# Kernel tuning notes

Hardware: AMD Instinct MI355X
Metric: run time of the kernel (lower is better)

The kernel has to match this reference:

```python
import jax, jax.numpy as jnp
import numpy as np

D_MODEL = 768
H = 12
D_FF = 3072
EPS = 1e-6


def _layernorm(x, alpha, bias):
    # torch.std default is Bessel-corrected (ddof=1); denom is (std + eps)
    mean = jnp.mean(x, axis=-1, keepdims=True)
    var = jnp.sum((x - mean) ** 2, axis=-1, keepdims=True) / (x.shape[-1] - 1)
    std = jnp.sqrt(var)
    return alpha * (x - mean) / (std + EPS) + bias


def _linear(x, w, b):
    # torch nn.Linear: y = x @ W.T + b, W is [out, in]
    return jnp.einsum('...i,oi->...o', x, w) + b


def setup_inputs() -> dict:
    key = jax.random.key(0)
    ks = jax.random.split(key, 16)
    B, S = 8, 1024
    sc = 1.0 / np.sqrt(D_MODEL)
    inp = {
        'x': jax.random.normal(ks[0], (B, S, D_MODEL), dtype=jnp.float32),
        'mask': jax.random.randint(ks[1], (B, 1, 1, S), 0, 2, dtype=jnp.int32),
        'wq': jax.random.normal(ks[2], (D_MODEL, D_MODEL), dtype=jnp.float32) * sc,
        'bq': jnp.zeros((D_MODEL,), jnp.float32),
        'wk': jax.random.normal(ks[3], (D_MODEL, D_MODEL), dtype=jnp.float32) * sc,
        'bk': jnp.zeros((D_MODEL,), jnp.float32),
        'wv': jax.random.normal(ks[4], (D_MODEL, D_MODEL), dtype=jnp.float32) * sc,
        'bv': jnp.zeros((D_MODEL,), jnp.float32),
        'wo': jax.random.normal(ks[5], (D_MODEL, D_MODEL), dtype=jnp.float32) * sc,
        'bo': jnp.zeros((D_MODEL,), jnp.float32),
        'ln1_a': jnp.ones((D_MODEL,), jnp.float32),
        'ln1_b': jnp.zeros((D_MODEL,), jnp.float32),
        'ln2_a': jnp.ones((D_MODEL,), jnp.float32),
        'ln2_b': jnp.zeros((D_MODEL,), jnp.float32),
        'w1': jax.random.normal(ks[6], (D_FF, D_MODEL), dtype=jnp.float32) * sc,
        'b1': jnp.zeros((D_FF,), jnp.float32),
        'w2': jax.random.normal(ks[7], (D_MODEL, D_FF), dtype=jnp.float32) * (1.0 / np.sqrt(D_FF)),
        'b2': jnp.zeros((D_MODEL,), jnp.float32),
    }
    return inp


def reference(x, mask, wq, bq, wk, bk, wv, bv, wo, bo,
              ln1_a, ln1_b, ln2_a, ln2_b, w1, b1, w2, b2):
    B, S, _ = x.shape
    d_k = D_MODEL // H

    # --- residual 1: pre-LN self-attention (dropout identity at eval) ---
    xn = _layernorm(x, ln1_a, ln1_b)
    q = _linear(xn, wq, bq).reshape(B, S, H, d_k).transpose(0, 2, 1, 3)
    k = _linear(xn, wk, bk).reshape(B, S, H, d_k).transpose(0, 2, 1, 3)
    v = _linear(xn, wv, bv).reshape(B, S, H, d_k).transpose(0, 2, 1, 3)

    scores = jnp.einsum('bhqd,bhkd->bhqk', q, k) / jnp.sqrt(jnp.float32(d_k))
    # faithful quirk: masked positions set to 1e-9, NOT -inf
    scores = jnp.where(mask == 0, jnp.float32(1e-9), scores)
    attn = jax.nn.softmax(scores, axis=-1)
    ctx = jnp.einsum('bhqk,bhkd->bhqd', attn, v)
    ctx = ctx.transpose(0, 2, 1, 3).reshape(B, S, D_MODEL)
    x = x + _linear(ctx, wo, bo)

    # --- residual 2: pre-LN feed-forward ---
    xn = _layernorm(x, ln2_a, ln2_b)
    ff = _linear(jax.nn.relu(_linear(xn, w1, b1)), w2, b2)
    return x + ff
```

## Files before the change

### kernel.cpp

```cpp
#include <hip/hip_runtime.h>
#include <stdint.h>

#define D_MODEL 768
#define D_FF    3072
#define NH      12
#define DK      64
#define BB      8
#define SS      1024
#define NTOK    (BB*SS)
#define QST     2304

typedef float          f32x4  __attribute__((ext_vector_type(4)));
typedef __bf16         bf16x8 __attribute__((ext_vector_type(8)));
typedef unsigned short us8v   __attribute__((ext_vector_type(8)));
typedef unsigned short us4v   __attribute__((ext_vector_type(4)));

__device__ __forceinline__ unsigned short f2b(float f) {
  unsigned int u = __builtin_bit_cast(unsigned int, f);
  u = (u + 0x7fffu + ((u >> 16) & 1u)) >> 16;
  return (unsigned short)u;
}
__device__ __forceinline__ float b2f(unsigned short h) {
  unsigned int u = ((unsigned int)h) << 16;
  return __builtin_bit_cast(float, u);
}
__device__ __forceinline__ float exp2a(float x) {
  float r; asm("v_exp_f32 %0, %1" : "=v"(r) : "v"(x)); return r;
}
__device__ __forceinline__ unsigned int cvtpk(float lo, float hi) {
  unsigned int r;
  asm("v_cvt_pk_bf16_f32 %0, %1, %2" : "=v"(r) : "v"(lo), "v"(hi));
  return r;
}

__global__ __launch_bounds__(256) void cast_kernel(const float* __restrict__ src,
                                                   unsigned short* __restrict__ dst,
                                                   int n4) {
  int i = blockIdx.x * 256 + threadIdx.x;
  if (i >= n4) return;
  const float4* s4 = (const float4*)src;
  float4 f = s4[i];
  us4v o; o.x = f2b(f.x); o.y = f2b(f.y); o.z = f2b(f.z); o.w = f2b(f.w);
  *(us4v*)(dst + (size_t)i * 4) = o;
}

__global__ __launch_bounds__(256) void ln_kernel(const float* __restrict__ x,
                                                 const float* __restrict__ ga,
                                                 const float* __restrict__ gb,
                                                 unsigned short* __restrict__ y) {
  int row = blockIdx.x;
  const float* xr = x + (size_t)row * D_MODEL;
  int t = threadIdx.x, w = t >> 6, l = t & 63;
  float v0 = xr[t], v1 = xr[t + 256], v2 = xr[t + 512];
  float s = v0 + v1 + v2;
  #pragma unroll
  for (int off = 32; off; off >>= 1) s += __shfl_xor(s, off);
  __shared__ float red[4];
  __shared__ float stats[2];
  if (l == 0) red[w] = s;
  __syncthreads();
  if (t == 0) stats[0] = (red[0] + red[1] + red[2] + red[3]) * (1.0f / 768.0f);
  __syncthreads();
  float mean = stats[0];
  float d0 = v0 - mean, d1 = v1 - mean, d2 = v2 - mean;
  float ss = d0 * d0 + d1 * d1 + d2 * d2;
  #pragma unroll
  for (int off = 32; off; off >>= 1) ss += __shfl_xor(ss, off);
  __syncthreads();
  if (l == 0) red[w] = ss;
  __syncthreads();
  if (t == 0) {
    float tot = red[0] + red[1] + red[2] + red[3];
    stats[1] = 1.0f / (sqrtf(tot * (1.0f / 767.0f)) + 1e-6f);
  }
  __syncthreads();
  float inv = stats[1];
  unsigned short* yr = y + (size_t)row * D_MODEL;
  yr[t]       = f2b(ga[t]       * (d0 * inv) + gb[t]);
  yr[t + 256] = f2b(ga[t + 256] * (d1 * inv) + gb[t + 256]);
  yr[t + 512] = f2b(ga[t + 512] * (d2 * inv) + gb[t + 512]);
}

#define GLDS(g, l) __builtin_amdgcn_global_load_lds( \
    (__attribute__((address_space(1))) const void*)(g), \
    (__attribute__((address_space(3))) void*)(l), 16, 0, 0)

template<int BN>
__global__ __launch_bounds__(256) void gemm_t(
    const unsigned short* __restrict__ A,
    const unsigned short* __restrict__ W,
    const float* __restrict__ biasA,
    const float* __restrict__ biasB,
    const float* __restrict__ biasC,
    int segw,
    const float* __restrict__ resid,
    float* __restrict__ outF,
    unsigned short* __restrict__ outB,
    int M, int N, int K, int relu) {
  constexpr int WC = (BN == 128) ? 2 : 1;
  constexpr int MF = (BN == 128) ? 4 : 2;
  constexpr int NF = 4;
  __shared__ unsigned short As[128 * 32];
  __shared__ unsigned short Bs[BN * 32];
  int t = threadIdx.x;
  int w = t >> 6, l = t & 63;
  int brow = blockIdx.x * 128;
  int bcol = blockIdx.y * BN;
  int wr = (w / WC) * (MF * 16);
  int wc = (w % WC) * (NF * 16);

  const unsigned short* ga0 = A + (size_t)(brow + (t >> 2)) * K + (t & 3) * 8;
  const unsigned short* ga1 = ga0 + (size_t)64 * K;
  const unsigned short* gb0 = W + (size_t)(bcol + (t >> 2)) * K + (t & 3) * 8;
  const unsigned short* gb1 = gb0 + (size_t)64 * K;

  f32x4 acc[MF][NF];
  #pragma unroll
  for (int m = 0; m < MF; m++)
    #pragma unroll
    for (int n = 0; n < NF; n++)
      acc[m][n] = (f32x4){0.f, 0.f, 0.f, 0.f};

  int arow = wr + (l & 15);
  int bcw  = wc + (l & 15);
  int kk   = (l >> 4) * 8;

  for (int k0 = 0; k0 < K; k0 += 32) {
    GLDS(ga0 + k0, As + t * 8);
    GLDS(ga1 + k0, As + 2048 + t * 8);
    GLDS(gb0 + k0, Bs + t * 8);
    if (BN == 128) GLDS(gb1 + k0, Bs + 2048 + t * 8);
    __syncthreads();
    bf16x8 af[MF], bfv[NF];
    #pragma unroll
    for (int m = 0; m < MF; m++)
      af[m] = *(const bf16x8*)(As + (arow + m * 16) * 32 + kk);
    #pragma unroll
    for (int n = 0; n < NF; n++)
      bfv[n] = *(const bf16x8*)(Bs + (bcw + n * 16) * 32 + kk);
    #pragma unroll
    for (int m = 0; m < MF; m++)
      #pragma unroll
      for (int n = 0; n < NF; n++)
        acc[m][n] = __builtin_amdgcn_mfma_f32_16x16x32_bf16(af[m], bfv[n], acc[m][n], 0, 0, 0);
    __syncthreads();
  }

  #pragma unroll
  for (int n = 0; n < NF; n++) {
    int col = bcol + wc + n * 16 + (l & 15);
    int seg = col / segw, off = col - seg * segw;
    const float* bp = (seg == 0) ? biasA : ((seg == 1) ? biasB : biasC);
    float bv = bp[off];
    #pragma unroll
    for (int m = 0; m < MF; m++) {
      int row0 = brow + wr + m * 16 + (l >> 4) * 4;
      #pragma unroll
      for (int r = 0; r < 4; r++) {
        int row = row0 + r;
        float vacc = acc[m][n][r] + bv;
        if (resid) vacc += resid[(size_t)row * N + col];
        if (relu)  vacc = fmaxf(vacc, 0.f);
        if (outF)  outF[(size_t)row * N + col] = vacc;
        if (outB)  outB[(size_t)row * N + col] = f2b(vacc);
      }
    }
  }
}

#define PPAD 72
#define KPAD 72
#define SM_C1 0.18033688011112043f
#define SM_C2 1.4426950408889634e-9f

__global__ __launch_bounds__(256) void attn_mfma(
    const unsigned short* __restrict__ qkv,
    const int* __restrict__ mask,
    unsigned short* __restrict__ ctx) {
  int bh = blockIdx.x;
  int qt = blockIdx.y;
  int b = bh / NH, h = bh % NH;
  int t = threadIdx.x, w = t >> 6, l = t & 63;
  int ql = l & 15, g = l >> 4;

  const unsigned short* kp = qkv + 768 + h * DK;
  const unsigned short* vp = qkv + 1536 + h * DK;

  __shared__ unsigned short Ks[4096];
  __shared__ unsigned short Vt[64 * KPAD];
  __shared__ unsigned short Ps[128 * PPAD];
  __shared__ float mk01[64];
  __shared__ float corrw[4][2][16];
  __shared__ float lrw[4][2][16];

  int srow = t >> 3;
  int sblk = t & 7;
  int sb0  = sblk ^ (srow & 7);
  int sb1  = sblk ^ ((srow + 32) & 7);

  bf16x8 qf[2][2];
  {
    const unsigned short* qp = qkv + h * DK;
    size_t row0 = (size_t)(b * SS + qt * 128 + w * 32 + ql);
    #pragma unroll
    for (int s = 0; s < 2; s++)
      #pragma unroll
      for (int ks = 0; ks < 2; ks++)
        qf[s][ks] = *(const bf16x8*)(qp + (row0 + s * 16) * QST + ks * 32 + g * 8);
  }

  f32x4 acc_o[2][4];
  #pragma unroll
  for (int s = 0; s < 2; s++)
    #pragma unroll
    for (int nf = 0; nf < 4; nf++) acc_o[s][nf] = (f32x4){0.f, 0.f, 0.f, 0.f};
  float mrun[2] = {-INFINITY, -INFINITY};
  float lrun[2] = {0.f, 0.f};

  for (int kt = 0; kt < 16; kt++) {
    size_t tok0 = (size_t)(b * SS + kt * 64);
    GLDS(kp + (tok0 + srow)      * QST + sb0 * 8, Ks + t * 8);
    GLDS(kp + (tok0 + srow + 32) * QST + sb1 * 8, Ks + 2048 + t * 8);
    {
      const unsigned short* vsrc = vp + (tok0 + l) * QST + w * 16;
      us8v v0 = *(const us8v*)vsrc;
      us8v v1 = *(const us8v*)(vsrc + 8);
      #pragma unroll
      for (int j = 0; j < 8; j++) {
        Vt[(w * 16 + j)     * KPAD + l] = v0[j];
        Vt[(w * 16 + 8 + j) * KPAD + l] = v1[j];
      }
    }
    if (t < 64) mk01[t] = mask[b * SS + kt * 64 + t] ? 1.0f : 0.0f;
    __syncthreads();

    f32x4 sa[2][4];
    #pragma unroll
    for (int s = 0; s < 2; s++)
      #pragma unroll
      for (int kf = 0; kf < 4; kf++) sa[s][kf] = (f32x4){0.f, 0.f, 0.f, 0.f};
    #pragma unroll
    for (int ks = 0; ks < 2; ks++) {
      bf16x8 kfr[4];
      #pragma unroll
      for (int kf = 0; kf < 4; kf++) {
        int row = kf * 16 + ql;
        kfr[kf] = *(const bf16x8*)(Ks + row * 64 + ((g + 4 * ks) ^ (ql & 7)) * 8);
      }
      #pragma unroll
      for (int s = 0; s < 2; s++)
        #pragma unroll
        for (int kf = 0; kf < 4; kf++)
          sa[s][kf] = __builtin_amdgcn_mfma_f32_16x16x32_bf16(kfr[kf], qf[s][ks], sa[s][kf], 0, 0, 0);
    }

    #pragma unroll
    for (int s = 0; s < 2; s++) {
      float pv[16];
      float tm = -INFINITY;
      #pragma unroll
      for (int kf = 0; kf < 4; kf++)
        #pragma unroll
        for (int r = 0; r < 4; r++) {
          float m01 = mk01[kf * 16 + g * 4 + r];
          float xm = sa[s][kf][r] * SM_C1 - SM_C2;
          float sc = fmaf(m01, xm, SM_C2);
          pv[kf * 4 + r] = sc;
          tm = fmaxf(tm, sc);
        }
      tm = fmaxf(tm, __shfl_xor(tm, 16));
      tm = fmaxf(tm, __shfl_xor(tm, 32));
      float mn = fmaxf(mrun[s], tm);
      float corr = exp2a(mrun[s] - mn);
      float rs = 0.f;
      #pragma unroll
      for (int i = 0; i < 16; i++) { pv[i] = exp2a(pv[i] - mn); rs += pv[i]; }
      rs += __shfl_xor(rs, 16);
      rs += __shfl_xor(rs, 32);
      mrun[s] = mn;
      lrun[s] = lrun[s] * corr + rs;

      int prow = w * 32 + s * 16 + ql;
      #pragma unroll
      for (int kf = 0; kf < 4; kf++) {
        uint2 pk;
        pk.x = cvtpk(pv[kf * 4 + 0], pv[kf * 4 + 1]);
        pk.y = cvtpk(pv[kf * 4 + 2], pv[kf * 4 + 3]);
        *(uint2*)(Ps + prow * PPAD + kf * 16 + g * 4) = pk;
      }
      if (l < 16) corrw[w][s][l] = corr;
    }

    #pragma unroll
    for (int s = 0; s < 2; s++) {
      float cb0 = corrw[w][s][g * 4 + 0], cb1 = corrw[w][s][g * 4 + 1];
      float cb2 = corrw[w][s][g * 4 + 2], cb3 = corrw[w][s][g * 4 + 3];
      #pragma unroll
      for (int nf = 0; nf < 4; nf++) {
        acc_o[s][nf][0] *= cb0; acc_o[s][nf][1] *= cb1;
        acc_o[s][nf][2] *= cb2; acc_o[s][nf][3] *= cb3;
      }
    }
    #pragma unroll
    for (int ks = 0; ks < 2; ks++) {
      bf16x8 vfr[4];
      #pragma unroll
      for (int nf = 0; nf < 4; nf++)
        vfr[nf] = *(const bf16x8*)(Vt + (ql + nf * 16) * KPAD + g * 8 + ks * 32);
      #pragma unroll
      for (int s = 0; s < 2; s++) {
        bf16x8 pa = *(const bf16x8*)(Ps + (w * 32 + s * 16 + ql) * PPAD + g * 8 + ks * 32);
        #pragma unroll
        for (int nf = 0; nf < 4; nf++)
          acc_o[s][nf] = __builtin_amdgcn_mfma_f32_16x16x32_bf16(pa, vfr[nf], acc_o[s][nf], 0, 0, 0);
      }
    }
    __syncthreads();
  }

  #pragma unroll
  for (int s = 0; s < 2; s++)
    if (l < 16) lrw[w][s][l] = lrun[s];
  #pragma unroll
  for (int s = 0; s < 2; s++) {
    float li0 = 1.0f / lrw[w][s][g * 4 + 0], li1 = 1.0f / lrw[w][s][g * 4 + 1];
    float li2 = 1.0f / lrw[w][s][g * 4 + 2], li3 = 1.0f / lrw[w][s][g * 4 + 3];
    #pragma unroll
    for (int nf = 0; nf < 4; nf++) {
      #pragma unroll
      for (int r = 0; r < 4; r++) {
        float li = (r == 0) ? li0 : (r == 1) ? li1 : (r == 2) ? li2 : li3;
        int tok = b * SS + qt * 128 + w * 32 + s * 16 + g * 4 + r;
        ctx[(size_t)tok * D_MODEL + h * DK + nf * 16 + ql] = f2b(acc_o[s][nf][r] * li);
      }
    }
  }
}

extern "C" void kernel_launch(void* const* d_in, const int* in_sizes, int n_in,
                              void* d_out, int out_size, void* d_ws, size_t ws_size,
                              hipStream_t stream) {
  const float* x    = (const float*)d_in[0];
  const int*   mask = (const int*)d_in[1];
  const float* wq   = (const float*)d_in[2];
  const float* bq   = (const float*)d_in[3];
  const float* wk   = (const float*)d_in[4];
  const float* bk   = (const float*)d_in[5];
  const float* wv   = (const float*)d_in[6];
  const float* bv   = (const float*)d_in[7];
  const float* wo   = (const float*)d_in[8];
  const float* bo   = (const float*)d_in[9];
  const float* ln1a = (const float*)d_in[10];
  const float* ln1b = (const float*)d_in[11];
  const float* ln2a = (const float*)d_in[12];
  const float* ln2b = (const float*)d_in[13];
  const float* w1   = (const float*)d_in[14];
  const float* b1   = (const float*)d_in[15];
  const float* w2   = (const float*)d_in[16];
  const float* b2   = (const float*)d_in[17];

  char* ws = (char*)d_ws;
  unsigned short* wqkvb = (unsigned short*)(ws + 0);
  unsigned short* wob   = (unsigned short*)(ws + 3538944);
  unsigned short* w1b   = (unsigned short*)(ws + 4718592);
  unsigned short* w2b   = (unsigned short*)(ws + 9437184);
  unsigned short* xnb   = (unsigned short*)(ws + 14155776);
  unsigned short* qkvb  = (unsigned short*)(ws + 26738688);
  unsigned short* ctxb  = (unsigned short*)(ws + 64487424);
  float*          x1    = (float*)(ws + 26738688);
  unsigned short* h1b   = (unsigned short*)(ws + 51904512);

  cast_kernel<<<(147456 + 255) / 256, 256, 0, stream>>>(wq, wqkvb, 147456);
  cast_kernel<<<(147456 + 255) / 256, 256, 0, stream>>>(wk, wqkvb + 589824, 147456);
  cast_kernel<<<(147456 + 255) / 256, 256, 0, stream>>>(wv, wqkvb + 1179648, 147456);
  cast_kernel<<<(147456 + 255) / 256, 256, 0, stream>>>(wo, wob, 147456);
  cast_kernel<<<(589824 + 255) / 256, 256, 0, stream>>>(w1, w1b, 589824);
  cast_kernel<<<(589824 + 255) / 256, 256, 0, stream>>>(w2, w2b, 589824);

  ln_kernel<<<NTOK, 256, 0, stream>>>(x, ln1a, ln1b, xnb);

  dim3 gqkv(NTOK / 128, QST / 128);
  gemm_t<128><<<gqkv, 256, 0, stream>>>(xnb, wqkvb, bq, bk, bv, 768,
                                        nullptr, nullptr, qkvb,
                                        NTOK, QST, D_MODEL, 0);

  dim3 ga(BB * NH, SS / 128);
  attn_mfma<<<ga, 256, 0, stream>>>(qkvb, mask, ctxb);

  dim3 gwo(NTOK / 128, D_MODEL / 64);
  gemm_t<64><<<gwo, 256, 0, stream>>>(ctxb, wob, bo, nullptr, nullptr, D_MODEL,
                                      x, x1, nullptr,
                                      NTOK, D_MODEL, D_MODEL, 0);

  ln_kernel<<<NTOK, 256, 0, stream>>>(x1, ln2a, ln2b, xnb);

  dim3 gff(NTOK / 128, D_FF / 128);
  gemm_t<128><<<gff, 256, 0, stream>>>(xnb, w1b, b1, nullptr, nullptr, D_FF,
                                       nullptr, nullptr, h1b,
                                       NTOK, D_FF, D_MODEL, 1);

  dim3 gff2(NTOK / 128, D_MODEL / 64);
  gemm_t<64><<<gff2, 256, 0, stream>>>(h1b, w2b, b2, nullptr, nullptr, D_MODEL,
                                       x1, (float*)d_out, nullptr,
                                       NTOK, D_MODEL, D_FF, 0);
}
```

Measured before the change: 314.6 us.

## Multi-buffer GEMM shared-memory tiles and merge weight casts into one kernel

Adds double buffering (BN=128) and triple buffering (BN=64) to the GEMM's LDS tiles. The next K-tile's global-to-LDS loads are issued before the MFMAs on the current tile, with vmcnt waits and a single barrier per iteration. This aims to hide global load latency behind compute. Separately, the six weight cast launches are fused into one kernel to cut launch overhead. The extra buffers raise LDS use per block and may lower occupancy, and the manual vmcnt accounting assumes a fixed number of outstanding loads per stage.

```diff
diff --git a/kernel.cpp b/kernel.cpp
--- a/kernel.cpp
+++ b/kernel.cpp
@@ -32,16 +32,33 @@
   asm("v_cvt_pk_bf16_f32 %0, %1, %2" : "=v"(r) : "v"(lo), "v"(hi));
   return r;
 }
-
-__global__ __launch_bounds__(256) void cast_kernel(const float* __restrict__ src,
-                                                   unsigned short* __restrict__ dst,
-                                                   int n4) {
+__device__ __forceinline__ void waitv3() {
+  asm volatile("s_waitcnt vmcnt(3)" ::: "memory");
+}
+__device__ __forceinline__ void waitv0() {
+  asm volatile("s_waitcnt vmcnt(0)" ::: "memory");
+}
+
+#define N4TOT 1769472
+__global__ __launch_bounds__(256) void cast6_kernel(
+    const float* __restrict__ s0, const float* __restrict__ s1,
+    const float* __restrict__ s2, const float* __restrict__ s3,
+    const float* __restrict__ s4, const float* __restrict__ s5,
+    unsigned short* __restrict__ d0, unsigned short* __restrict__ d1,
+    unsigned short* __restrict__ d2, unsigned short* __restrict__ d3,
+    unsigned short* __restrict__ d4, unsigned short* __restrict__ d5) {
   int i = blockIdx.x * 256 + threadIdx.x;
-  if (i >= n4) return;
-  const float4* s4 = (const float4*)src;
-  float4 f = s4[i];
+  if (i >= N4TOT) return;
+  const float* src; unsigned short* dst; int off;
+  if (i < 147456)       { src = s0; dst = d0; off = i; }
+  else if (i < 294912)  { src = s1; dst = d1; off = i - 147456; }
+  else if (i < 442368)  { src = s2; dst = d2; off = i - 294912; }
+  else if (i < 589824)  { src = s3; dst = d3; off = i - 442368; }
+  else if (i < 1179648) { src = s4; dst = d4; off = i - 589824; }
+  else                  { src = s5; dst = d5; off = i - 1179648; }
+  float4 f = ((const float4*)src)[off];
   us4v o; o.x = f2b(f.x); o.y = f2b(f.y); o.z = f2b(f.z); o.w = f2b(f.w);
-  *(us4v*)(dst + (size_t)i * 4) = o;
+  *(us4v*)(dst + (size_t)off * 4) = o;
 }
 
 __global__ __launch_bounds__(256) void ln_kernel(const float* __restrict__ x,
@@ -100,8 +117,11 @@
   constexpr int WC = (BN == 128) ? 2 : 1;
   constexpr int MF = (BN == 128) ? 4 : 2;
   constexpr int NF = 4;
-  __shared__ unsigned short As[128 * 32];
-  __shared__ unsigned short Bs[BN * 32];
+  constexpr int NBUF = (BN == 128) ? 2 : 3;
+  constexpr int ASZ = 128 * 32;
+  constexpr int BSZ = BN * 32;
+  __shared__ unsigned short As[NBUF * ASZ];
+  __shared__ unsigned short Bs[NBUF * BSZ];
   int t = threadIdx.x;
   int w = t >> 6, l = t & 63;
   int brow = blockIdx.x * 128;
@@ -124,26 +144,58 @@
   int arow = wr + (l & 15);
   int bcw  = wc + (l & 15);
   int kk   = (l >> 4) * 8;
-
-  for (int k0 = 0; k0 < K; k0 += 32) {
-    GLDS(ga0 + k0, As + t * 8);
-    GLDS(ga1 + k0, As + 2048 + t * 8);
-    GLDS(gb0 + k0, Bs + t * 8);
-    if (BN == 128) GLDS(gb1 + k0, Bs + 2048 + t * 8);
+  const int nt = K / 32;
+
+  auto stage = [&](int ti, int buf) {
+    int k0 = ti * 32;
+    GLDS(ga0 + k0, As + buf * ASZ + t * 8);
+    GLDS(ga1 + k0, As + buf * ASZ + 2048 + t * 8);
+    GLDS(gb0 + k0, Bs + buf * BSZ + t * 8);
+    if constexpr (BN == 128) GLDS(gb1 + k0, Bs + buf * BSZ + 2048 + t * 8);
+  };
+
+  if constexpr (NBUF == 3) {
+    stage(0, 0);
+    stage(1, 1);
+    waitv3();
+    __builtin_amdgcn_s_barrier();
+    __builtin_amdgcn_sched_barrier(0);
+  } else {
+    stage(0, 0);
     __syncthreads();
+  }
+
+  int cb = 0, sb = 2;
+  for (int ti = 0; ti < nt; ti++) {
+    if constexpr (NBUF == 3) {
+      if (ti + 2 < nt) { stage(ti + 2, sb); sb = (sb == 2) ? 0 : sb + 1; }
+    } else {
+      if (ti + 1 < nt) stage(ti + 1, cb ^ 1);
+    }
     bf16x8 af[MF], bfv[NF];
     #pragma unroll
     for (int m = 0; m < MF; m++)
-      af[m] = *(const bf16x8*)(As + (arow + m * 16) * 32 + kk);
+      af[m] = *(const bf16x8*)(As + cb * ASZ + (arow + m * 16) * 32 + kk);
     #pragma unroll
     for (int n = 0; n < NF; n++)
-      bfv[n] = *(const bf16x8*)(Bs + (bcw + n * 16) * 32 + kk);
+      bfv[n] = *(const bf16x8*)(Bs + cb * BSZ + (bcw + n * 16) * 32 + kk);
     #pragma unroll
     for (int m = 0; m < MF; m++)
       #pragma unroll
       for (int n = 0; n < NF; n++)
         acc[m][n] = __builtin_amdgcn_mfma_f32_16x16x32_bf16(af[m], bfv[n], acc[m][n], 0, 0, 0);
-    __syncthreads();
+    if constexpr (NBUF == 3) {
+      if (ti + 2 < nt)      waitv3();
+      else if (ti + 1 < nt) waitv0();
+      if (ti + 1 < nt) {
+        __builtin_amdgcn_s_barrier();
+        __builtin_amdgcn_sched_barrier(0);
+      }
+      cb = (cb == 2) ? 0 : cb + 1;
+    } else {
+      if (ti + 1 < nt) __syncthreads();
+      cb ^= 1;
+    }
   }
 
   #pragma unroll
@@ -370,12 +422,9 @@
   float*          x1    = (float*)(ws + 26738688);
   unsigned short* h1b   = (unsigned short*)(ws + 51904512);
 
-  cast_kernel<<<(147456 + 255) / 256, 256, 0, stream>>>(wq, wqkvb, 147456);
-  cast_kernel<<<(147456 + 255) / 256, 256, 0, stream>>>(wk, wqkvb + 589824, 147456);
-  cast_kernel<<<(147456 + 255) / 256, 256, 0, stream>>>(wv, wqkvb + 1179648, 147456);
-  cast_kernel<<<(147456 + 255) / 256, 256, 0, stream>>>(wo, wob, 147456);
-  cast_kernel<<<(589824 + 255) / 256, 256, 0, stream>>>(w1, w1b, 589824);
-  cast_kernel<<<(589824 + 255) / 256, 256, 0, stream>>>(w2, w2b, 589824);
+  cast6_kernel<<<N4TOT / 256, 256, 0, stream>>>(
+      wq, wk, wv, wo, w1, w2,
+      wqkvb, wqkvb + 589824, wqkvb + 1179648, wob, w1b, w2b);
 
   ln_kernel<<<NTOK, 256, 0, stream>>>(x, ln1a, ln1b, xnb);
 
```

Measured after the change: 297.3 us. 5.5% less time.
